# Kernel optimization log

Hardware: AMD Instinct MI355X
Metric: run time of the kernel (lower is better)

The kernel has to match this reference:

```python
import jax, jax.numpy as jnp
import numpy as np

ROI_SIZE = 14  # hard-coded in the torch module


def _bilinear(feature, x, y):
    """feature: [B,C,H,W]; x, y: arbitrary (matching) shape S of sample coords.
    Returns [B, C, *S]. Matches torch code: corner indices are clamped BEFORE
    the interpolation weights are computed from them."""
    H, W = feature.shape[-2:]
    y1 = jnp.clip(jnp.floor(y).astype(jnp.int32), 0, H - 1)
    y2 = jnp.clip(jnp.floor(y).astype(jnp.int32) + 1, 0, H - 1)
    x1 = jnp.clip(jnp.floor(x).astype(jnp.int32), 0, W - 1)
    x2 = jnp.clip(jnp.floor(x).astype(jnp.int32) + 1, 0, W - 1)
    wx_lo = x - x1  # weight toward x2 column
    wx_hi = x2 - x  # weight toward x1 column
    wy_lo = y - y1
    wy_hi = y2 - y
    p = feature[:, :, y1, x1] * wx_hi + feature[:, :, y1, x2] * wx_lo
    q = feature[:, :, y2, x1] * wx_hi + feature[:, :, y2, x2] * wx_lo
    return p * wy_hi + q * wy_lo


def setup_inputs() -> dict:
    key = jax.random.key(0)
    kf, k1, k2, k3, k4 = jax.random.split(key, 5)
    B, C, H, W, R = 1, 256, 200, 320, 128
    feature = jax.random.normal(kf, (B, C, H, W), dtype=jnp.float32)
    y1 = jax.random.uniform(k1, (R,), minval=0.0, maxval=H * 0.5)
    x1 = jax.random.uniform(k2, (R,), minval=0.0, maxval=W * 0.5)
    hh = jax.random.uniform(k3, (R,), minval=8.0, maxval=H * 0.45)
    ww = jax.random.uniform(k4, (R,), minval=8.0, maxval=W * 0.45)
    rois = jnp.stack([y1, x1, y1 + hh, x1 + ww], axis=-1).astype(jnp.float32)
    return {"feature": feature, "rois": rois}


def reference(feature, rois):
    R = rois.shape[0]
    B, C, H, W = feature.shape
    sh = (rois[:, 2] - rois[:, 0]) / ROI_SIZE  # [R] bin height stride
    sw = (rois[:, 3] - rois[:, 1]) / ROI_SIZE  # [R] bin width stride
    m = jnp.arange(ROI_SIZE, dtype=rois.dtype)
    y_base = rois[:, 0:1] + sh[:, None] * m  # [R, M]
    x_base = rois[:, 1:2] + sw[:, None] * m  # [R, N]
    frac = jnp.array([1.0 / 3.0, 2.0 / 3.0], dtype=rois.dtype)
    ys = y_base[:, :, None] + sh[:, None, None] * frac  # [R, M, 2]
    xs = x_base[:, :, None] + sw[:, None, None] * frac  # [R, N, 2]
    # all 4 (y, x) sample-point combos per bin -> [R, M, N, 2, 2]
    yy = jnp.broadcast_to(ys[:, :, None, :, None], (R, ROI_SIZE, ROI_SIZE, 2, 2))
    xx = jnp.broadcast_to(xs[:, None, :, None, :], (R, ROI_SIZE, ROI_SIZE, 2, 2))
    samples = _bilinear(feature, xx, yy)  # [B, C, R, M, N, 2, 2]
    # Faithful to torch.max(tensor) with NO dim: global max over B, C, R and
    # the 4 sample points, giving one scalar per bin (m, n).
    bin_max = jnp.max(samples, axis=(0, 1, 2, 5, 6))  # [M, N]
    return jnp.broadcast_to(bin_max, (R, C, ROI_SIZE, ROI_SIZE))
```

## Files before the change

kernel.cpp:

```cpp
#include <hip/hip_runtime.h>
#include <float.h>
#include <stdint.h>

#define CC 256
#define HH 200
#define WW 320
#define HW (HH * WW)
#define MM 14
#define NCH 4
#define CG 4
#define CPB (CC / CG)
#define NR (CPB / NCH)
#define SP4 38
#define SPF (SP4 * 4)

__global__ void roi_init(float* __restrict__ binmax) {
    int t = blockIdx.x * blockDim.x + threadIdx.x;
    if (t < MM * MM) binmax[t] = -FLT_MAX;
}

__device__ inline void atomicMaxF(float* addr, float val) {
    if (val >= 0.0f) {
        atomicMax((int*)addr, __float_as_int(val));
    } else {
        atomicMin((unsigned int*)addr, __float_as_uint(val));
    }
}

__device__ __forceinline__ void gload_lds16(const float* g, float* l) {
    __builtin_amdgcn_global_load_lds(
        (const __attribute__((address_space(1))) unsigned int*)g,
        (__attribute__((address_space(3))) unsigned int*)l,
        16, 0, 0);
}

__global__ __launch_bounds__(256, 8) void roi_reduce(
    const float* __restrict__ feature,
    const float* __restrict__ rois,
    float* __restrict__ binmax)
{
    const int bid = blockIdx.x;
    const int cg  = bid & (CG - 1);
    const int rm  = bid >> 2;
    const int m   = rm % MM;
    const int r   = rm / MM;
    const int tid = threadIdx.x;
    const int cbase = cg * CPB;

    const float ry1 = rois[r * 4 + 0];
    const float rx1 = rois[r * 4 + 1];
    const float ry2 = rois[r * 4 + 2];
    const float rx2 = rois[r * 4 + 3];
    const float sh = (ry2 - ry1) * (1.0f / 14.0f);
    const float sw = (rx2 - rx1) * (1.0f / 14.0f);
    const float f13 = 1.0f / 3.0f, f23 = 2.0f / 3.0f;

    const float yA = ry1 + sh * (float)m + sh * f13;
    const float yB = ry1 + sh * (float)m + sh * f23;
    const int y1A = min(max((int)floorf(yA), 0), HH - 1);
    const int y2A = min(max((int)floorf(yA) + 1, 0), HH - 1);
    const int y1B = min(max((int)floorf(yB), 0), HH - 1);
    const int y2B = min(max((int)floorf(yB) + 1, 0), HH - 1);
    const float wyloA = yA - (float)y1A, wyhiA = (float)y2A - yA;
    const float wyloB = yB - (float)y1B, wyhiB = (float)y2B - yB;

    const float xmin = rx1 + sw * f13;
    const float xmax = rx1 + sw * 13.0f + sw * f23;
    int xlo = min(max((int)floorf(xmin), 0), WW - 1);
    int xhi = min(max((int)floorf(xmax) + 1, 0), WW - 1);
    const int xlo4 = xlo & ~3;
    int span = xhi - xlo4 + 1;
    if (span > 4 * SP4 - 4) span = 4 * SP4 - 4;
    const int span4 = (span + 3) >> 2;

    const int s  = tid % 56;
    const int cs = tid / 56;
    const int n  = s >> 2;
    const int j  = (s >> 1) & 1;
    const int i  = s & 1;
    const bool active = (tid < 224);

    float wxlo = 0.f, wxhi = 0.f, wylo = 0.f, wyhi = 0.f;
    int c0 = 0, c1 = 0, ra = 0, rb = 1;
    if (active) {
        float x = rx1 + sw * (float)n + sw * (j ? f23 : f13);
        int x1c = min(max((int)floorf(x), 0), WW - 1);
        int x2c = min(max((int)floorf(x) + 1, 0), WW - 1);
        wxlo = x - (float)x1c;
        wxhi = (float)x2c - x;
        c0 = min(max(x1c - xlo4, 0), span - 1);
        c1 = min(max(x2c - xlo4, 0), span - 1);
        if (i == 0) { ra = 0; rb = 1; wylo = wyloA; wyhi = wyhiA; }
        else        { ra = 2; rb = 3; wylo = wyloB; wyhi = wyhiB; }
    }

    __shared__ float tileF[2][NCH][4][SPF];
    float* pmax = &tileF[0][0][0][0];

    const int rg   = tid >> 6;
    const int lane = tid & 63;
    const int myrow = (rg == 0) ? y1A : (rg == 1) ? y2A : (rg == 2) ? y1B : y2B;
    const float* gRow = feature + cbase * HW + myrow * WW + xlo4 + (lane << 2);
    const bool ld = lane < span4;

    if (ld) {
        const float* g = gRow;
        #pragma unroll
        for (int ch = 0; ch < NCH; ++ch) {
            gload_lds16(g, &tileF[0][ch][rg][0]);
            g += HW;
        }
    }

    float lmax = -FLT_MAX;
    for (int r8 = 0; r8 < NR; ++r8) {
        const int b = r8 & 1;
        if (r8 + 1 < NR) {
            if (ld) {
                const float* g = gRow + (r8 + 1) * NCH * HW;
                #pragma unroll
                for (int ch = 0; ch < NCH; ++ch) {
                    gload_lds16(g, &tileF[b ^ 1][ch][rg][0]);
                    g += HW;
                }
            }
            asm volatile("s_waitcnt vmcnt(4)" ::: "memory");
        } else {
            asm volatile("s_waitcnt vmcnt(0)" ::: "memory");
        }
        __builtin_amdgcn_s_barrier();
        asm volatile("" ::: "memory");

        if (active) {
            const float* ta = &tileF[b][cs][ra][0];
            const float* tb = &tileF[b][cs][rb][0];
            float v11 = ta[c0], v12 = ta[c1];
            float v21 = tb[c0], v22 = tb[c1];
            float p  = v11 * wxhi + v12 * wxlo;
            float q2 = v21 * wxhi + v22 * wxlo;
            lmax = fmaxf(lmax, p * wyhi + q2 * wylo);
        }

        asm volatile("s_waitcnt lgkmcnt(0)" ::: "memory");
        __builtin_amdgcn_s_barrier();
        asm volatile("" ::: "memory");
    }

    if (active) pmax[tid] = lmax;
    __syncthreads();
    if (tid < MM) {
        float v = -FLT_MAX;
        #pragma unroll
        for (int c4 = 0; c4 < 4; ++c4)
            #pragma unroll
            for (int q4 = 0; q4 < 4; ++q4)
                v = fmaxf(v, pmax[c4 * 56 + tid * 4 + q4]);
        atomicMaxF(&binmax[m * MM + tid], v);
    }
}

__global__ __launch_bounds__(256) void roi_bcast(
    const float* __restrict__ binmax, float4* __restrict__ out, int total4)
{
    __shared__ float4 b4[49];
    int t = threadIdx.x;
    if (t < 49) b4[t] = ((const float4*)binmax)[t];
    __syncthreads();
    const int stride = gridDim.x * 256;
    for (int idx = blockIdx.x * 256 + t; idx < total4; idx += stride)
        out[idx] = b4[idx % 49];
}

extern "C" void kernel_launch(void* const* d_in, const int* in_sizes, int n_in,
                              void* d_out, int out_size, void* d_ws, size_t ws_size,
                              hipStream_t stream) {
    const float* feature = (const float*)d_in[0];
    const float* rois    = (const float*)d_in[1];
    float* binmax = (float*)d_ws;
    float* out    = (float*)d_out;

    const int R = in_sizes[1] / 4;

    roi_init<<<1, 256, 0, stream>>>(binmax);
    roi_reduce<<<R * MM * CG, 256, 0, stream>>>(feature, rois, binmax);

    const int total4 = out_size / 4;
    int nb = (total4 + 255) / 256;
    if (nb > 2048) nb = 2048;
    roi_bcast<<<nb, 256, 0, stream>>>(binmax, (float4*)out, total4);
}
```

Before: 162.4 us.

## Give each wave private channels and LDS buffers to drop block barriers

Each of the four waves in a block now owns a contiguous slice of channels and loads all four feature rows itself into its own double-buffered LDS region. Previously the four waves split by row and shared the buffers, so every loop iteration needed two block-wide barriers. Waves now synchronise only through their own vmcnt/lgkmcnt waits, and the loop is unrolled by two to alternate buffers. Total loads and LDS size stay the same; the cost is more address setup per wave and less cross-wave staggering of memory requests.

Measured after the change: 182.9 us. 12.6% more time.

```diff
diff --git a/kernel.cpp b/kernel.cpp
--- a/kernel.cpp
+++ b/kernel.cpp
@@ -7,10 +7,9 @@
 #define WW 320
 #define HW (HH * WW)
 #define MM 14
-#define NCH 4
 #define CG 4
 #define CPB (CC / CG)
-#define NR (CPB / NCH)
+#define KPW (CPB / 4)
 #define SP4 38
 #define SPF (SP4 * 4)
 
@@ -45,7 +44,9 @@
     const int m   = rm % MM;
     const int r   = rm / MM;
     const int tid = threadIdx.x;
-    const int cbase = cg * CPB;
+    const int w    = tid >> 6;
+    const int lane = tid & 63;
+    const int cbase = cg * CPB + w * KPW;
 
     const float ry1 = rois[r * 4 + 0];
     const float rx1 = rois[r * 4 + 1];
@@ -73,12 +74,10 @@
     if (span > 4 * SP4 - 4) span = 4 * SP4 - 4;
     const int span4 = (span + 3) >> 2;
 
-    const int s  = tid % 56;
-    const int cs = tid / 56;
-    const int n  = s >> 2;
-    const int j  = (s >> 1) & 1;
-    const int i  = s & 1;
-    const bool active = (tid < 224);
+    const int n = lane >> 2;
+    const int j = (lane >> 1) & 1;
+    const int i = lane & 1;
+    const bool active = (lane < 56);
 
     float wxlo = 0.f, wxhi = 0.f, wylo = 0.f, wyhi = 0.f;
     int c0 = 0, c1 = 0, ra = 0, rb = 1;
@@ -94,67 +93,69 @@
         else        { ra = 2; rb = 3; wylo = wyloB; wyhi = wyhiB; }
     }
 
-    __shared__ float tileF[2][NCH][4][SPF];
-    float* pmax = &tileF[0][0][0][0];
+    __shared__ float tileF[4][2][4][SPF];
+    float* ldsW = &tileF[w][0][0][0];
 
-    const int rg   = tid >> 6;
-    const int lane = tid & 63;
-    const int myrow = (rg == 0) ? y1A : (rg == 1) ? y2A : (rg == 2) ? y1B : y2B;
-    const float* gRow = feature + cbase * HW + myrow * WW + xlo4 + (lane << 2);
+    const float* gBase = feature + (size_t)cbase * HW + xlo4 + (lane << 2);
+    const int o0 = y1A * WW, o1 = y2A * WW, o2 = y1B * WW, o3 = y2B * WW;
     const bool ld = lane < span4;
 
-    if (ld) {
-        const float* g = gRow;
-        #pragma unroll
-        for (int ch = 0; ch < NCH; ++ch) {
-            gload_lds16(g, &tileF[0][ch][rg][0]);
-            g += HW;
-        }
-    }
+    const float* p0a = ldsW + 0 * 4 * SPF + ra * SPF;
+    const float* p0b = ldsW + 0 * 4 * SPF + rb * SPF;
+    const float* p1a = ldsW + 1 * 4 * SPF + ra * SPF;
+    const float* p1b = ldsW + 1 * 4 * SPF + rb * SPF;
 
+    #define STAGE(kk, bb) do { if (ld) {                                  \
+        const float* g_ = gBase + (size_t)(kk) * HW;                      \
+        gload_lds16(g_ + o0, ldsW + (bb) * 4 * SPF + 0 * SPF);            \
+        gload_lds16(g_ + o1, ldsW + (bb) * 4 * SPF + 1 * SPF);            \
+        gload_lds16(g_ + o2, ldsW + (bb) * 4 * SPF + 2 * SPF);            \
+        gload_lds16(g_ + o3, ldsW + (bb) * 4 * SPF + 3 * SPF); } } while (0)
+
+    STAGE(0, 0);
     float lmax = -FLT_MAX;
-    for (int r8 = 0; r8 < NR; ++r8) {
-        const int b = r8 & 1;
-        if (r8 + 1 < NR) {
-            if (ld) {
-                const float* g = gRow + (r8 + 1) * NCH * HW;
-                #pragma unroll
-                for (int ch = 0; ch < NCH; ++ch) {
-                    gload_lds16(g, &tileF[b ^ 1][ch][rg][0]);
-                    g += HW;
-                }
-            }
+
+    for (int k = 0; k < KPW; k += 2) {
+        asm volatile("s_waitcnt lgkmcnt(0)" ::: "memory");
+        if (k + 1 < KPW) {
+            STAGE(k + 1, 1);
             asm volatile("s_waitcnt vmcnt(4)" ::: "memory");
         } else {
             asm volatile("s_waitcnt vmcnt(0)" ::: "memory");
         }
-        __builtin_amdgcn_s_barrier();
-        asm volatile("" ::: "memory");
-
-        if (active) {
-            const float* ta = &tileF[b][cs][ra][0];
-            const float* tb = &tileF[b][cs][rb][0];
-            float v11 = ta[c0], v12 = ta[c1];
-            float v21 = tb[c0], v22 = tb[c1];
+        {
+            float v11 = p0a[c0], v12 = p0a[c1];
+            float v21 = p0b[c0], v22 = p0b[c1];
             float p  = v11 * wxhi + v12 * wxlo;
             float q2 = v21 * wxhi + v22 * wxlo;
             lmax = fmaxf(lmax, p * wyhi + q2 * wylo);
         }
+        asm volatile("s_waitcnt lgkmcnt(0)" ::: "memory");
+        if (k + 2 < KPW) {
+            STAGE(k + 2, 0);
+            asm volatile("s_waitcnt vmcnt(4)" ::: "memory");
+        } else {
+            asm volatile("s_waitcnt vmcnt(0)" ::: "memory");
+        }
+        {
+            float v11 = p1a[c0], v12 = p1a[c1];
+            float v21 = p1b[c0], v22 = p1b[c1];
+            float p  = v11 * wxhi + v12 * wxlo;
+            float q2 = v21 * wxhi + v22 * wxlo;
+            lmax = fmaxf(lmax, p * wyhi + q2 * wylo);
+        }
+    }
+    #undef STAGE
 
-        asm volatile("s_waitcnt lgkmcnt(0)" ::: "memory");
-        __builtin_amdgcn_s_barrier();
-        asm volatile("" ::: "memory");
-    }
-
-    if (active) pmax[tid] = lmax;
+    if (active) ldsW[lane] = lmax;
     __syncthreads();
     if (tid < MM) {
         float v = -FLT_MAX;
         #pragma unroll
-        for (int c4 = 0; c4 < 4; ++c4)
+        for (int w4 = 0; w4 < 4; ++w4)
             #pragma unroll
             for (int q4 = 0; q4 < 4; ++q4)
-                v = fmaxf(v, pmax[c4 * 56 + tid * 4 + q4]);
+                v = fmaxf(v, tileF[w4][0][0][tid * 4 + q4]);
         atomicMaxF(&binmax[m * MM + tid], v);
     }
 }
```

## Replace double-buffered LDS pipeline with single-buffer 8-channel batches

Applied to the files above, without the earlier changes.

Drops the two-stage double-buffered global-to-LDS prefetch and its explicit waitcnt/barrier handling. Each iteration now loads 8 channels into a single LDS buffer, synchronizes, and each thread processes two channels per iteration. This halves the number of loop iterations and barriers per block and keeps the LDS footprint about the same, but loads no longer overlap with compute inside a block. Overlap now has to come from other resident blocks.

Result: no change. 162.2 us (-0.2%).

```diff
diff --git a/kernel.cpp b/kernel.cpp
--- a/kernel.cpp
+++ b/kernel.cpp
@@ -7,10 +7,9 @@
 #define WW 320
 #define HW (HH * WW)
 #define MM 14
-#define NCH 4
+#define NCH 8
 #define CG 4
 #define CPB (CC / CG)
-#define NR (CPB / NCH)
 #define SP4 38
 #define SPF (SP4 * 4)
 
@@ -94,8 +93,8 @@
         else        { ra = 2; rb = 3; wylo = wyloB; wyhi = wyhiB; }
     }
 
-    __shared__ float tileF[2][NCH][4][SPF];
-    float* pmax = &tileF[0][0][0][0];
+    __shared__ float tileF[NCH][4][SPF];
+    __shared__ float pmax[224];
 
     const int rg   = tid >> 6;
     const int lane = tid & 63;
@@ -103,47 +102,32 @@
     const float* gRow = feature + cbase * HW + myrow * WW + xlo4 + (lane << 2);
     const bool ld = lane < span4;
 
-    if (ld) {
-        const float* g = gRow;
-        #pragma unroll
-        for (int ch = 0; ch < NCH; ++ch) {
-            gload_lds16(g, &tileF[0][ch][rg][0]);
-            g += HW;
+    float lmax = -FLT_MAX;
+
+    for (int cc = 0; cc < CPB; cc += NCH) {
+        __syncthreads();
+        if (ld) {
+            const float* g = gRow + (size_t)cc * HW;
+            #pragma unroll
+            for (int ch = 0; ch < NCH; ++ch) {
+                gload_lds16(g, &tileF[ch][rg][0]);
+                g += HW;
+            }
         }
-    }
-
-    float lmax = -FLT_MAX;
-    for (int r8 = 0; r8 < NR; ++r8) {
-        const int b = r8 & 1;
-        if (r8 + 1 < NR) {
-            if (ld) {
-                const float* g = gRow + (r8 + 1) * NCH * HW;
-                #pragma unroll
-                for (int ch = 0; ch < NCH; ++ch) {
-                    gload_lds16(g, &tileF[b ^ 1][ch][rg][0]);
-                    g += HW;
-                }
+        __syncthreads();
+        if (active) {
+            #pragma unroll
+            for (int q = 0; q < 2; ++q) {
+                const int ch = cs * 2 + q;
+                float v11 = tileF[ch][ra][c0];
+                float v12 = tileF[ch][ra][c1];
+                float v21 = tileF[ch][rb][c0];
+                float v22 = tileF[ch][rb][c1];
+                float p  = v11 * wxhi + v12 * wxlo;
+                float q2 = v21 * wxhi + v22 * wxlo;
+                lmax = fmaxf(lmax, p * wyhi + q2 * wylo);
             }
-            asm volatile("s_waitcnt vmcnt(4)" ::: "memory");
-        } else {
-            asm volatile("s_waitcnt vmcnt(0)" ::: "memory");
         }
-        __builtin_amdgcn_s_barrier();
-        asm volatile("" ::: "memory");
-
-        if (active) {
-            const float* ta = &tileF[b][cs][ra][0];
-            const float* tb = &tileF[b][cs][rb][0];
-            float v11 = ta[c0], v12 = ta[c1];
-            float v21 = tb[c0], v22 = tb[c1];
-            float p  = v11 * wxhi + v12 * wxlo;
-            float q2 = v21 * wxhi + v22 * wxlo;
-            lmax = fmaxf(lmax, p * wyhi + q2 * wylo);
-        }
-
-        asm volatile("s_waitcnt lgkmcnt(0)" ::: "memory");
-        __builtin_amdgcn_s_barrier();
-        asm volatile("" ::: "memory");
     }
 
     if (active) pmax[tid] = lmax;
```
